# Optimization experiments

Measured on AMD Instinct MI355X. Metric: run time of the kernel, lower is better.

Reference implementation:

```python
import jax, jax.numpy as jnp
import numpy as np

HEADS = 4


def _forward(x_atoms, pos, edge_attr, molecular_features, emb_W, emb_b, mp_W1, mp_b1, mp_W2, mp_b2, ln_g, ln_b, attn_in_w, attn_in_b, attn_out_w, attn_out_b, pool_W, pool_b, mol_gate, lrn_gate, molemb_W1, molemb_b1, molemb_W2, molemb_b2, lrnemb_W1, lrnemb_b1, lrnemb_W2, lrnemb_b2, fus_W1, fus_b1, fus_W2, fus_b2, head_W1, head_b1, head_W2, head_b2, edge_index, batch_idx):
    N = x_atoms.shape[0]
    B = molecular_features.shape[0]
    A = N // B  # equal-size molecules; batch_idx = repeat(arange(B), A)
    H = emb_W.shape[1]
    L = mp_W1.shape[0]
    src, dst = edge_index[0], edge_index[1]  # PyG: x_j = x[src], x_i = x[dst]
    x = x_atoms @ emb_W + emb_b
    # distance features (constant across layers)
    diff = pos[dst] - pos[src]
    d = jnp.sqrt(jnp.sum(diff * diff, axis=1, keepdims=True) + 1e-12)
    dist_feat = jnp.concatenate([d, 1.0 / (1.0 + d), jnp.exp(-d)], axis=1)  # [E,3]
    ones_e = jnp.ones((src.shape[0], 1), x.dtype)
    cnt = jnp.maximum(jax.ops.segment_sum(ones_e, dst, num_segments=N), 1.0)
    for l in range(L):
        res = x
        msg = jnp.concatenate([x[dst], x[src], dist_feat], axis=1)  # [E, 2H+3]
        msg = jax.nn.relu(msg @ mp_W1[l] + mp_b1[l]) @ mp_W2[l] + mp_b2[l]
        x = jax.ops.segment_sum(msg, dst, num_segments=N) / cnt  # mean aggregation
        y = x + res
        mu = y.mean(-1, keepdims=True)
        var = jnp.var(y, axis=-1, keepdims=True)
        x = (y - mu) * jax.lax.rsqrt(var + 1e-5) * ln_g[l] + ln_b[l]
    xm = x.reshape(B, A, H)
    explicit = xm.mean(axis=1)  # scatter_mean over equal-size graphs
    # per-molecule multi-head self-attention (torch MHA, eval mode)
    hd = H // HEADS
    qkv = xm @ attn_in_w.T + attn_in_b
    q, k, v = jnp.split(qkv, 3, axis=-1)
    q = q.reshape(B, A, HEADS, hd)
    k = k.reshape(B, A, HEADS, hd)
    v = v.reshape(B, A, HEADS, hd)
    scores = jnp.einsum('bqhd,bkhd->bhqk', q, k) / jnp.sqrt(jnp.asarray(hd, x.dtype))
    att = jax.nn.softmax(scores, axis=-1)
    o = jnp.einsum('bhqk,bkhd->bqhd', att, v).reshape(B, A, H)
    attended = o @ attn_out_w.T + attn_out_b
    aw = jax.nn.softmax(jnp.sum(attended * xm, axis=-1), axis=1)  # [B,A]
    wmean = jnp.sum(attended * aw[..., None], axis=1)
    maxp = attended.max(axis=1)
    meanp = attended.mean(axis=1)
    stdp = jnp.std(attended, axis=1, ddof=1)  # torch.std unbiased
    pooled = jnp.stack([wmean, maxp, meanp, stdp], axis=0)  # [4,B,H]
    proj = jnp.einsum('kbh,khf->kbf', pooled, pool_W) + pool_b[:, None, :]
    learned = jnp.moveaxis(proj, 0, 1).reshape(B, -1)  # [B,LF]
    # per-property gated MLPs, vectorized over P (atom gates are computed but unused in the source)
    gm = molecular_features[None] * jax.nn.sigmoid(mol_gate)[:, None, :]
    gl = learned[None] * jax.nn.sigmoid(lrn_gate)[:, None, :]
    molrep = jax.nn.relu(jnp.einsum('pbm,pmh->pbh', gm, molemb_W1) + molemb_b1[:, None, :])
    molrep = jnp.einsum('pbh,phk->pbk', molrep, molemb_W2) + molemb_b2[:, None, :]
    lrnrep = jax.nn.relu(jnp.einsum('pbm,pmh->pbh', gl, lrnemb_W1) + lrnemb_b1[:, None, :])
    lrnrep = jnp.einsum('pbh,phk->pbk', lrnrep, lrnemb_W2) + lrnemb_b2[:, None, :]
    P = mol_gate.shape[0]
    comb = jnp.concatenate([jnp.broadcast_to(explicit[None], (P, B, H)), molrep, lrnrep], axis=-1)
    fused = jax.nn.relu(jnp.einsum('pbc,pch->pbh', comb, fus_W1) + fus_b1[:, None, :])
    fused = jnp.einsum('pbh,phk->pbk', fused, fus_W2) + fus_b2[:, None, :]
    h = jax.nn.relu(jnp.einsum('pbh,phk->pbk', fused, head_W1) + head_b1[:, None, :])
    out = jnp.einsum('pbk,pko->pbo', h, head_W2) + head_b2[:, None, :]
    return out  # [P,B,1]: stacked predictions for the 4 properties


def setup_inputs() -> dict:
    key = jax.random.key(0)
    ks = jax.random.split(key, 24)
    B, A, F, M, H, LF, L, P = 1024, 32, 64, 200, 128, 64, 3, 4
    N = B * A
    E = N * 16
    H2, H4, Q = H // 2, H // 4, LF // 4
    n = lambda i, shape, s=1.0: jax.random.normal(ks[i], shape, dtype=jnp.float32) * s
    inp = {}
    inp['x_atoms'] = n(0, (N, F))
    inp['pos'] = n(1, (N, 3)) * 3.0
    inp['edge_attr'] = n(2, (E, 4))
    inp['molecular_features'] = n(3, (B, M))
    inp['emb_W'] = n(4, (F, H), 0.1)
    inp['emb_b'] = jnp.zeros((H,), jnp.float32)
    inp['mp_W1'] = n(5, (L, 2 * H + 3, H), 0.05)
    inp['mp_b1'] = jnp.zeros((L, H), jnp.float32)
    inp['mp_W2'] = n(6, (L, H, H), 0.05)
    inp['mp_b2'] = jnp.zeros((L, H), jnp.float32)
    inp['ln_g'] = jnp.ones((L, H), jnp.float32)
    inp['ln_b'] = jnp.zeros((L, H), jnp.float32)
    inp['attn_in_w'] = n(7, (3 * H, H), 0.08)
    inp['attn_in_b'] = jnp.zeros((3 * H,), jnp.float32)
    inp['attn_out_w'] = n(8, (H, H), 0.08)
    inp['attn_out_b'] = jnp.zeros((H,), jnp.float32)
    inp['pool_W'] = n(9, (4, H, Q), 0.08)
    inp['pool_b'] = jnp.zeros((4, Q), jnp.float32)
    inp['mol_gate'] = n(10, (P, M))
    inp['lrn_gate'] = n(11, (P, LF))
    inp['molemb_W1'] = n(12, (P, M, H2), 0.08)
    inp['molemb_b1'] = jnp.zeros((P, H2), jnp.float32)
    inp['molemb_W2'] = n(13, (P, H2, H2), 0.08)
    inp['molemb_b2'] = jnp.zeros((P, H2), jnp.float32)
    inp['lrnemb_W1'] = n(14, (P, LF, H2), 0.08)
    inp['lrnemb_b1'] = jnp.zeros((P, H2), jnp.float32)
    inp['lrnemb_W2'] = n(15, (P, H2, H2), 0.08)
    inp['lrnemb_b2'] = jnp.zeros((P, H2), jnp.float32)
    inp['fus_W1'] = n(16, (P, 2 * H, H), 0.08)
    inp['fus_b1'] = jnp.zeros((P, H), jnp.float32)
    inp['fus_W2'] = n(17, (P, H, H2), 0.08)
    inp['fus_b2'] = jnp.zeros((P, H2), jnp.float32)
    inp['head_W1'] = n(18, (P, H2, H4), 0.08)
    inp['head_b1'] = jnp.zeros((P, H4), jnp.float32)
    inp['head_W2'] = n(19, (P, H4, 1), 0.08)
    inp['head_b2'] = jnp.zeros((P, 1), jnp.float32)
    inp['edge_index'] = jax.random.randint(ks[20], (2, E), 0, N)
    inp['batch_idx'] = jnp.repeat(jnp.arange(B), A)
    return inp


def reference(x_atoms, pos, edge_attr, molecular_features, emb_W, emb_b, mp_W1, mp_b1, mp_W2, mp_b2, ln_g, ln_b, attn_in_w, attn_in_b, attn_out_w, attn_out_b, pool_W, pool_b, mol_gate, lrn_gate, molemb_W1, molemb_b1, molemb_W2, molemb_b2, lrnemb_W1, lrnemb_b1, lrnemb_W2, lrnemb_b2, fus_W1, fus_b1, fus_W2, fus_b2, head_W1, head_b1, head_W2, head_b2, edge_index, batch_idx):
    return _forward(x_atoms, pos, edge_attr, molecular_features, emb_W, emb_b, mp_W1, mp_b1, mp_W2, mp_b2, ln_g, ln_b, attn_in_w, attn_in_b, attn_out_w, attn_out_b, pool_W, pool_b, mol_gate, lrn_gate, molemb_W1, molemb_b1, molemb_W2, molemb_b2, lrnemb_W1, lrnemb_b1, lrnemb_W2, lrnemb_b2, fus_W1, fus_b1, fus_W2, fus_b2, head_W1, head_b1, head_W2, head_b2, edge_index, batch_idx)
```

## Files before the change

### kernel.cpp

```cpp
#include <hip/hip_runtime.h>

#define NE 524288
#define NN 32768
#define NB 1024

#define F4(p) (*(const float4*)(p))

typedef __bf16 bf16x8 __attribute__((ext_vector_type(8)));
typedef float  f32x4  __attribute__((ext_vector_type(4)));

__device__ __forceinline__ float sigmoidf_(float v) { return 1.f / (1.f + expf(-v)); }

__device__ __forceinline__ void bf16split(float f, short &hi, short &lo) {
  unsigned u = __float_as_uint(f);
  unsigned rh = (u + 0x7FFFu + ((u >> 16) & 1u)) >> 16;
  float fh = __uint_as_float(rh << 16);
  float fl = f - fh;
  unsigned u2 = __float_as_uint(fl);
  unsigned rl = (u2 + 0x7FFFu + ((u2 >> 16) & 1u)) >> 16;
  hi = (short)rh; lo = (short)rl;
}

__device__ __forceinline__ unsigned short f2bf(float f) {
  unsigned u = __float_as_uint(f);
  return (unsigned short)((u + 0x7FFFu + ((u >> 16) & 1u)) >> 16);
}
__device__ __forceinline__ float bf2f(unsigned short h) {
  return __uint_as_float(((unsigned)h) << 16);
}

__device__ __forceinline__ void ld32(float* xr, const float* p) {
#pragma unroll
  for (int i = 0; i < 32; i += 4) {
    float4 v = F4(&p[i]);
    xr[i] = v.x; xr[i+1] = v.y; xr[i+2] = v.z; xr[i+3] = v.w;
  }
}

__device__ __forceinline__ float dot32r(const float* __restrict__ w, const float* xr) {
  float s = 0.f;
#pragma unroll
  for (int i = 0; i < 32; i += 4) {
    float4 ww = F4(&w[i]);
    s = fmaf(xr[i],   ww.x, s);
    s = fmaf(xr[i+1], ww.y, s);
    s = fmaf(xr[i+2], ww.z, s);
    s = fmaf(xr[i+3], ww.w, s);
  }
  return s;
}

__global__ __launch_bounds__(128) void embed_kernel(
    const float* __restrict__ xa, const float* __restrict__ W,
    const float* __restrict__ b, float* __restrict__ x)
{
  __shared__ float a[64];
  const int n = blockIdx.x, t = threadIdx.x;
  if (t < 64) a[t] = xa[n*64 + t];
  __syncthreads();
  float s = b[t];
#pragma unroll 8
  for (int f = 0; f < 64; ++f) s = fmaf(a[f], W[f*128 + t], s);
  x[n*128 + t] = s;
}

__global__ __launch_bounds__(256) void hist_kernel(const int* __restrict__ ei, int* __restrict__ cnt) {
  const int e = blockIdx.x*256 + threadIdx.x;
  atomicAdd(&cnt[ei[NE + e]], 1);
}

__global__ __launch_bounds__(1024) void scan_kernel(
    const int* __restrict__ cnt, int* __restrict__ off, int* __restrict__ cur)
{
  __shared__ int wsum[16];
  const int t = threadIdx.x;
  int local[32];
  const int base = t*32;
  int s = 0;
#pragma unroll
  for (int i = 0; i < 32; ++i) { local[i] = cnt[base+i]; s += local[i]; }
  int pre = s;
  const int lane = t & 63;
#pragma unroll
  for (int o = 1; o < 64; o <<= 1) { int v = __shfl_up(pre, o); if (lane >= o) pre += v; }
  if (lane == 63) wsum[t >> 6] = pre;
  __syncthreads();
  if (t == 0) { int a = 0; for (int w = 0; w < 16; ++w) { int v = wsum[w]; wsum[w] = a; a += v; } }
  __syncthreads();
  int excl = wsum[t >> 6] + pre - s;
#pragma unroll
  for (int i = 0; i < 32; ++i) { off[base+i] = excl; cur[base+i] = excl; excl += local[i]; }
  if (t == 1023) off[NN] = excl;
}

__global__ __launch_bounds__(256) void scatter_kernel(
    const float* __restrict__ pos, const int* __restrict__ ei,
    int* __restrict__ cur, float4* __restrict__ csr_rec)
{
  const int e = blockIdx.x*256 + threadIdx.x;
  const int s = ei[e];
  const int d = ei[NE + e];
  float dx = pos[d*3+0] - pos[s*3+0];
  float dy = pos[d*3+1] - pos[s*3+1];
  float dz = pos[d*3+2] - pos[s*3+2];
  float dist = sqrtf(dx*dx + dy*dy + dz*dz + 1e-12f);
  const int slot = atomicAdd(&cur[d], 1);
  csr_rec[slot] = make_float4(__int_as_float(s), dist, 1.f/(1.f + dist), expf(-dist));
}

__device__ __forceinline__ void pack_decode(int r, int N, int &k, int &n) {
  const int j = r & 7, lane = (r >> 3) & 63, rest = r >> 9;
  const int NT = N >> 4;
  const int t = rest % NT, kc = rest / NT;
  k = kc*32 + (lane >> 4)*8 + j;
  n = t*16 + (lane & 15);
}

#define W1AB_OFF 0
#define W2_OFF   98304
#define WIN_OFF  147456
#define WOUT_OFF 196608
#define HA_OFF   212992
#define HB_OFF   270336
#define HL_OFF   335872
#define HD_OFF   352256
#define HF1_OFF  417792
#define HF2_OFF  942080
#define HH1_OFF  1073152
#define PK_TOTAL 1105920

__global__ __launch_bounds__(256) void prep_kernel(
    const float* __restrict__ mp_W1, const float* __restrict__ mp_W2,
    const float* __restrict__ win, const float* __restrict__ wout,
    const float* __restrict__ mp_b1,
    const float* __restrict__ mol_gate, const float* __restrict__ lrn_gate,
    const float* __restrict__ meW1, const float* __restrict__ meW2,
    const float* __restrict__ leW1, const float* __restrict__ leW2,
    const float* __restrict__ fW1, const float* __restrict__ fW2,
    const float* __restrict__ hW1,
    short* __restrict__ bh, short* __restrict__ bl, float* __restrict__ pqbias)
{
  const int i = blockIdx.x*256 + threadIdx.x;
  if (i < 768) { const int l = i >> 8, t = i & 255; pqbias[i] = t < 128 ? mp_b1[l*128 + t] : 0.f; }
  if (i >= PK_TOTAL) return;
  int k, n; float v;
  if (i < W2_OFF) {
    const int l = i / 32768, r = i % 32768;
    pack_decode(r, 256, k, n);
    const float* W = mp_W1 + (size_t)l*259*128;
    v = (n < 128) ? W[k*128 + n] : W[(128+k)*128 + (n-128)];
  } else if (i < WIN_OFF) {
    const int q = i - W2_OFF, l = q / 16384, r = q % 16384;
    pack_decode(r, 128, k, n);
    v = mp_W2[(size_t)l*16384 + k*128 + n];
  } else if (i < WOUT_OFF) {
    pack_decode(i - WIN_OFF, 384, k, n);
    v = win[n*128 + k];
  } else if (i < HA_OFF) {
    pack_decode(i - WOUT_OFF, 128, k, n);
    v = wout[n*128 + k];
  } else if (i < HB_OFF) {
    pack_decode(i - HA_OFF, 256, k, n);
    const int p = n >> 6, h = n & 63;
    v = (k < 200) ? meW1[p*12800 + k*64 + h] * sigmoidf_(mol_gate[p*200 + k]) : 0.f;
  } else if (i < HL_OFF) {
    pack_decode(i - HB_OFF, 256, k, n);
    const int p = n >> 6, h = n & 63, kp = k >> 6, c = k & 63;
    v = (kp == p) ? meW2[p*4096 + c*64 + h] : 0.f;
  } else if (i < HD_OFF) {
    pack_decode(i - HL_OFF, 256, k, n);
    const int p = n >> 6, h = n & 63;
    v = leW1[p*4096 + k*64 + h] * sigmoidf_(lrn_gate[p*64 + k]);
  } else if (i < HF1_OFF) {
    pack_decode(i - HD_OFF, 256, k, n);
    const int p = n >> 6, h = n & 63, kp = k >> 6, c = k & 63;
    v = (kp == p) ? leW2[p*4096 + c*64 + h] : 0.f;
  } else if (i < HF2_OFF) {
    pack_decode(i - HF1_OFF, 512, k, n);
    const int p = n >> 7, h = n & 127, kp = k >> 8, c = k & 255;
    v = (kp == p) ? fW1[p*32768 + c*128 + h] : 0.f;
  } else if (i < HH1_OFF) {
    pack_decode(i - HF2_OFF, 256, k, n);
    const int p = n >> 6, h = n & 63, kp = k >> 7, c = k & 127;
    v = (kp == p) ? fW2[p*8192 + c*64 + h] : 0.f;
  } else {
    pack_decode(i - HH1_OFF, 128, k, n);
    const int p = n >> 5, h = n & 31, kp = k >> 6, c = k & 63;
    v = (kp == p) ? hW1[p*2048 + c*32 + h] : 0.f;
  }
  short h_, lo; bf16split(v, h_, lo);
  bh[i] = h_; bl[i] = lo;
}

__global__ __launch_bounds__(256, 2) void mfma_gemm_kernel(
    const float* __restrict__ A, int lda, int K,
    const short* __restrict__ Bh, const short* __restrict__ Bl,
    const float* __restrict__ bias, float* __restrict__ C, int ncols, int ldc,
    int colstride, int coloff, int relu,
    unsigned short* __restrict__ qbf)
{
  const int lane = threadIdx.x & 63, wid = threadIdx.x >> 6;
  const int m0 = blockIdx.x * 128 + wid * 32;
  const int n0 = blockIdx.y * 64;
  const int NT = ncols >> 4;
  const int cl = lane & 15, kg = lane >> 4;
  const int KC = K >> 5;

  f32x4 acc[2][4];
#pragma unroll
  for (int s = 0; s < 2; ++s)
#pragma unroll
    for (int t = 0; t < 4; ++t) acc[s][t] = (f32x4){0.f,0.f,0.f,0.f};

  for (int kc = 0; kc < KC; ++kc) {
    bf16x8 Ah[2], Al[2];
#pragma unroll
    for (int s = 0; s < 2; ++s) {
      const float* ap = &A[(size_t)(m0 + s*16 + cl)*lda + kc*32 + kg*8];
      const float4 f0 = F4(ap), f1 = F4(ap + 4);
      const float fv[8] = {f0.x,f0.y,f0.z,f0.w,f1.x,f1.y,f1.z,f1.w};
      union { short s[8]; bf16x8 b; } uh, ul;
#pragma unroll
      for (int j = 0; j < 8; ++j) bf16split(fv[j], uh.s[j], ul.s[j]);
      Ah[s] = uh.b; Al[s] = ul.b;
    }
    bf16x8 Bfh[4], Bfl[4];
#pragma unroll
    for (int t = 0; t < 4; ++t) {
      const size_t off = (((size_t)(kc*NT + (n0 >> 4) + t))*64 + lane)*8;
      Bfh[t] = *(const bf16x8*)&Bh[off];
      Bfl[t] = *(const bf16x8*)&Bl[off];
    }
#pragma unroll
    for (int s = 0; s < 2; ++s)
#pragma unroll
      for (int t = 0; t < 4; ++t)
        acc[s][t] = __builtin_amdgcn_mfma_f32_16x16x32_bf16(Ah[s], Bfh[t], acc[s][t], 0, 0, 0);
#pragma unroll
    for (int s = 0; s < 2; ++s)
#pragma unroll
      for (int t = 0; t < 4; ++t)
        acc[s][t] = __builtin_amdgcn_mfma_f32_16x16x32_bf16(Ah[s], Bfl[t], acc[s][t], 0, 0, 0);
#pragma unroll
    for (int s = 0; s < 2; ++s)
#pragma unroll
      for (int t = 0; t < 4; ++t)
        acc[s][t] = __builtin_amdgcn_mfma_f32_16x16x32_bf16(Al[s], Bfh[t], acc[s][t], 0, 0, 0);
  }

#pragma unroll
  for (int t = 0; t < 4; ++t) {
    const int col = n0 + t*16 + cl;
    const float bv = bias[col];
    const int dstcol = (col >> 6)*colstride + coloff + (col & 63);
#pragma unroll
    for (int s = 0; s < 2; ++s) {
      const int rbase = m0 + s*16 + kg*4;
#pragma unroll
      for (int r = 0; r < 4; ++r) {
        float v = acc[s][t][r] + bv;
        if (relu) v = fmaxf(v, 0.f);
        if (qbf && col >= 128)
          qbf[(size_t)(rbase + r)*128 + (col - 128)] = f2bf(v);
        else
          C[(size_t)(rbase + r)*ldc + dstcol] = v;
      }
    }
  }
}

__global__ __launch_bounds__(256, 2) void mfma_gemm_ln_kernel(
    const float* __restrict__ A, int lda,
    const short* __restrict__ Bh, const short* __restrict__ Bl,
    const float* __restrict__ b2, const int* __restrict__ csr_off,
    const float* __restrict__ g, const float* __restrict__ bb,
    float* __restrict__ x)
{
  const int lane = threadIdx.x & 63, wid = threadIdx.x >> 6;
  const int m0 = blockIdx.x * 64 + wid * 16;
  const int cl = lane & 15, kg = lane >> 4;

  bf16x8 Ah[4], Al[4];
#pragma unroll
  for (int kc = 0; kc < 4; ++kc) {
    const float* ap = &A[(size_t)(m0 + cl)*lda + kc*32 + kg*8];
    const float4 f0 = F4(ap), f1 = F4(ap + 4);
    const float fv[8] = {f0.x,f0.y,f0.z,f0.w,f1.x,f1.y,f1.z,f1.w};
    union { short s[8]; bf16x8 b; } uh, ul;
#pragma unroll
    for (int j = 0; j < 8; ++j) bf16split(fv[j], uh.s[j], ul.s[j]);
    Ah[kc] = uh.b; Al[kc] = ul.b;
  }

  f32x4 acc[8];
#pragma unroll
  for (int t = 0; t < 8; ++t) acc[t] = (f32x4){0.f,0.f,0.f,0.f};

#pragma unroll
  for (int kc = 0; kc < 4; ++kc) {
    bf16x8 Bfh[8], Bfl[8];
#pragma unroll
    for (int t = 0; t < 8; ++t) {
      const size_t off = (((size_t)(kc*8 + t))*64 + lane)*8;
      Bfh[t] = *(const bf16x8*)&Bh[off];
      Bfl[t] = *(const bf16x8*)&Bl[off];
    }
#pragma unroll
    for (int t = 0; t < 8; ++t)
      acc[t] = __builtin_amdgcn_mfma_f32_16x16x32_bf16(Ah[kc], Bfh[t], acc[t], 0, 0, 0);
#pragma unroll
    for (int t = 0; t < 8; ++t)
      acc[t] = __builtin_amdgcn_mfma_f32_16x16x32_bf16(Ah[kc], Bfl[t], acc[t], 0, 0, 0);
#pragma unroll
    for (int t = 0; t < 8; ++t)
      acc[t] = __builtin_amdgcn_mfma_f32_16x16x32_bf16(Al[kc], Bfh[t], acc[t], 0, 0, 0);
  }

  const int r0 = m0 + kg*4;
  float sflag[4];
#pragma unroll
  for (int r = 0; r < 4; ++r)
    sflag[r] = (csr_off[r0 + r + 1] > csr_off[r0 + r]) ? 1.f : 0.f;

  float ps[4] = {0.f,0.f,0.f,0.f}, pq[4] = {0.f,0.f,0.f,0.f};
  float yv[8][4];
#pragma unroll
  for (int t = 0; t < 8; ++t) {
    const int col = t*16 + cl;
    const float b2v = b2[col];
#pragma unroll
    for (int r = 0; r < 4; ++r) {
      const float y = acc[t][r] + sflag[r]*b2v + x[(size_t)(r0 + r)*128 + col];
      yv[t][r] = y;
      ps[r] += y;
      pq[r] = fmaf(y, y, pq[r]);
    }
  }
#pragma unroll
  for (int o = 1; o < 16; o <<= 1) {
#pragma unroll
    for (int r = 0; r < 4; ++r) { ps[r] += __shfl_xor(ps[r], o); pq[r] += __shfl_xor(pq[r], o); }
  }
#pragma unroll
  for (int r = 0; r < 4; ++r) {
    const float mu = ps[r] * (1.f/128.f);
    const float var = pq[r]*(1.f/128.f) - mu*mu;
    const float rstd = rsqrtf(var + 1e-5f);
#pragma unroll
    for (int t = 0; t < 8; ++t) {
      const int col = t*16 + cl;
      x[(size_t)(r0 + r)*128 + col] = (yv[t][r] - mu)*rstd*g[col] + bb[col];
    }
  }
}

__global__ __launch_bounds__(256, 6) void agg_kernel(
    float* __restrict__ P, const unsigned short* __restrict__ Qbf,
    const int* __restrict__ csr_off, const float4* __restrict__ csr_rec,
    const float* __restrict__ W1)
{
  const int tid = threadIdx.x;
  const int node = blockIdx.x*4 + (tid >> 6);
  const int lane = tid & 63;
  const int c0 = lane*2;
  const int off0 = csr_off[node], off1 = csr_off[node+1];

  const float* __restrict__ w1c = W1 + 256*128;
  const float w00 = w1c[c0],       w01 = w1c[c0+1];
  const float w10 = w1c[128+c0],   w11 = w1c[128+c0+1];
  const float w20 = w1c[256+c0],   w21 = w1c[256+c0+1];
  const float2 p = *(const float2*)&P[(size_t)node*128 + c0];

  float a0 = 0.f, a1 = 0.f;
  int e = off0;
  for (; e + 8 <= off1; e += 8) {
    float4 rc[8];
#pragma unroll
    for (int j = 0; j < 8; ++j) rc[j] = csr_rec[e+j];
    ushort2 qv[8];
#pragma unroll
    for (int j = 0; j < 8; ++j)
      qv[j] = *(const ushort2*)&Qbf[(size_t)__float_as_int(rc[j].x)*128 + c0];
#pragma unroll
    for (int j = 0; j < 8; ++j) {
      float h0 = p.x + bf2f(qv[j].x);
      h0 = fmaf(rc[j].y, w00, h0); h0 = fmaf(rc[j].z, w10, h0); h0 = fmaf(rc[j].w, w20, h0);
      float h1 = p.y + bf2f(qv[j].y);
      h1 = fmaf(rc[j].y, w01, h1); h1 = fmaf(rc[j].z, w11, h1); h1 = fmaf(rc[j].w, w21, h1);
      a0 += fmaxf(h0, 0.f);
      a1 += fmaxf(h1, 0.f);
    }
  }
  for (; e < off1; ++e) {
    const float4 rc = csr_rec[e];
    const ushort2 qv = *(const ushort2*)&Qbf[(size_t)__float_as_int(rc.x)*128 + c0];
    float h0 = p.x + bf2f(qv.x);
    h0 = fmaf(rc.y, w00, h0); h0 = fmaf(rc.z, w10, h0); h0 = fmaf(rc.w, w20, h0);
    float h1 = p.y + bf2f(qv.y);
    h1 = fmaf(rc.y, w01, h1); h1 = fmaf(rc.z, w11, h1); h1 = fmaf(rc.w, w21, h1);
    a0 += fmaxf(h0, 0.f);
    a1 += fmaxf(h1, 0.f);
  }
  const int deg = off1 - off0;
  const float rc_ = deg > 0 ? 1.f/(float)deg : 1.f;
  *(float2*)&P[(size_t)node*128 + c0] = make_float2(a0*rc_, a1*rc_);
}

__global__ __launch_bounds__(128) void attn_kernel(float* __restrict__ dqkv)
{
  __shared__ float sk[32*132];
  __shared__ float sv[32*132];
  const int tid = threadIdx.x;
  const int b = blockIdx.x;

  for (int idx = tid; idx < 1024; idx += 128) {
    const int a = idx >> 5, c4 = idx & 31;
    *(float4*)&sk[a*132 + c4*4] = F4(&dqkv[(size_t)(b*32+a)*384 + 128 + c4*4]);
    *(float4*)&sv[a*132 + c4*4] = F4(&dqkv[(size_t)(b*32+a)*384 + 256 + c4*4]);
  }
  __syncthreads();

  const int h = tid >> 5, qr = tid & 31;
  float qreg[32];
  ld32(qreg, &dqkv[(size_t)(b*32+qr)*384 + h*32]);

  float sc[32];
#pragma unroll
  for (int k = 0; k < 32; ++k)
    sc[k] = dot32r(&sk[k*132 + h*32], qreg) * 0.17677669529663687f;
  float mx = sc[0];
#pragma unroll
  for (int k = 1; k < 32; ++k) mx = fmaxf(mx, sc[k]);
  float se = 0.f;
#pragma unroll
  for (int k = 0; k < 32; ++k) { sc[k] = expf(sc[k] - mx); se += sc[k]; }
  const float inv = 1.f / se;

  __syncthreads();

  float od[32];
#pragma unroll
  for (int i = 0; i < 32; ++i) od[i] = 0.f;
#pragma unroll 4
  for (int k = 0; k < 32; ++k) {
    const float w = sc[k] * inv;
    const float* vr = &sv[k*132 + h*32];
#pragma unroll
    for (int i = 0; i < 32; i += 4) {
      float4 v = F4(&vr[i]);
      od[i]   = fmaf(w, v.x, od[i]);
      od[i+1] = fmaf(w, v.y, od[i+1]);
      od[i+2] = fmaf(w, v.z, od[i+2]);
      od[i+3] = fmaf(w, v.w, od[i+3]);
    }
  }
#pragma unroll
  for (int i = 0; i < 32; i += 4)
    *(float4*)&sk[qr*132 + h*32 + i] = make_float4(od[i], od[i+1], od[i+2], od[i+3]);
  __syncthreads();

  for (int idx = tid; idx < 1024; idx += 128) {
    const int a = idx >> 5, c4 = idx & 31;
    *(float4*)&dqkv[(size_t)(b*32+a)*384 + 256 + c4*4] = F4(&sk[a*132 + c4*4]);
  }
}

__global__ __launch_bounds__(128) void pool_kernel(
    const float* __restrict__ att, const float* __restrict__ x,
    const float* __restrict__ pW, const float* __restrict__ pb,
    float* __restrict__ expl, float* __restrict__ lrn, float* __restrict__ comb)
{
  __shared__ float satt[32*132];
  __shared__ float sx[32*132];
  __shared__ float aw_l[32];
  __shared__ float spool[512];
  const int tid = threadIdx.x;
  const int b = blockIdx.x;

  for (int idx = tid; idx < 1024; idx += 128) {
    const int a = idx >> 5, c4 = idx & 31;
    *(float4*)&satt[a*132 + c4*4] = F4(&att[(size_t)(b*32+a)*128 + c4*4]);
    *(float4*)&sx[a*132 + c4*4]   = F4(&x[(size_t)(b*32+a)*128 + c4*4]);
  }
  __syncthreads();

  {
    const int a = tid >> 2, q4 = tid & 3;
    float sp = 0.f;
#pragma unroll
    for (int i = 0; i < 32; ++i)
      sp = fmaf(satt[a*132 + q4*32 + i], sx[a*132 + q4*32 + i], sp);
    sp += __shfl_xor(sp, 1);
    sp += __shfl_xor(sp, 2);
    if (q4 == 0) aw_l[a] = sp;
  }
  __syncthreads();

  {
    float awr[32];
    float mxl = aw_l[0];
#pragma unroll
    for (int a = 1; a < 32; ++a) mxl = fmaxf(mxl, aw_l[a]);
    float se = 0.f;
#pragma unroll
    for (int a = 0; a < 32; ++a) { awr[a] = expf(aw_l[a] - mxl); se += awr[a]; }
    const float inv = 1.f / se;
    const int c = tid;
    float mx = -3.4e38f, sm = 0.f, wm = 0.f, ex = 0.f;
#pragma unroll
    for (int a = 0; a < 32; ++a) {
      const float v = satt[a*132 + c];
      mx = fmaxf(mx, v);
      sm += v;
      wm = fmaf(v, awr[a], wm);
      ex += sx[a*132 + c];
    }
    wm *= inv;
    const float mean = sm * 0.03125f;
    float s2 = 0.f;
#pragma unroll
    for (int a = 0; a < 32; ++a) {
      const float d = satt[a*132 + c] - mean;
      s2 = fmaf(d, d, s2);
    }
    const float stdp = sqrtf(s2 * (1.f/31.f));
    const float exm = ex * 0.03125f;
    expl[b*128 + c] = exm;
#pragma unroll
    for (int p = 0; p < 4; ++p)
      comb[(size_t)b*1024 + p*256 + c] = exm;
    spool[c]       = wm;
    spool[128 + c] = mx;
    spool[256 + c] = mean;
    spool[384 + c] = stdp;
  }
  __syncthreads();

  if (tid < 64) {
    const int k = tid >> 4, qq = tid & 15;
    const float* pk = pW + k*2048;
    float s0 = 0.f, s1 = 0.f, s2 = 0.f, s3 = 0.f;
    for (int h2 = 0; h2 < 128; h2 += 4) {
      s0 = fmaf(spool[k*128 + h2],   pk[h2*16 + qq],     s0);
      s1 = fmaf(spool[k*128 + h2+1], pk[(h2+1)*16 + qq], s1);
      s2 = fmaf(spool[k*128 + h2+2], pk[(h2+2)*16 + qq], s2);
      s3 = fmaf(spool[k*128 + h2+3], pk[(h2+3)*16 + qq], s3);
    }
    lrn[b*64 + tid] = pb[k*16 + qq] + (s0+s1) + (s2+s3);
  }
}

__global__ __launch_bounds__(256) void padmolf_kernel(
    const float* __restrict__ molf, float* __restrict__ mp)
{
  const int i = blockIdx.x*256 + threadIdx.x;
  const int b = i / 224, m = i - b*224;
  mp[i] = (m < 200) ? molf[b*200 + m] : 0.f;
}

__global__ __launch_bounds__(256) void outdot_kernel(
    const float* __restrict__ H1, const float* __restrict__ hW2,
    const float* __restrict__ hb2, float* __restrict__ out)
{
  const int id = blockIdx.x*256 + threadIdx.x;
  const int b = id & 1023, p = id >> 10;
  const float* hp = &H1[(size_t)b*128 + p*32];
  const float* wp = &hW2[p*32];
  float s0=0.f,s1=0.f,s2=0.f,s3=0.f;
  for (int h = 0; h < 32; h += 4) {
    s0 = fmaf(hp[h],   wp[h],   s0);
    s1 = fmaf(hp[h+1], wp[h+1], s1);
    s2 = fmaf(hp[h+2], wp[h+2], s2);
    s3 = fmaf(hp[h+3], wp[h+3], s3);
  }
  out[p*1024 + b] = (s0+s1) + (s2+s3) + hb2[p];
}

extern "C" void kernel_launch(void* const* d_in, const int* in_sizes, int n_in,
                              void* d_out, int out_size, void* d_ws, size_t ws_size,
                              hipStream_t stream) {
  const float* x_atoms    = (const float*)d_in[0];
  const float* pos        = (const float*)d_in[1];
  const float* molf       = (const float*)d_in[3];
  const float* emb_W      = (const float*)d_in[4];
  const float* emb_b      = (const float*)d_in[5];
  const float* mp_W1      = (const float*)d_in[6];
  const float* mp_b1      = (const float*)d_in[7];
  const float* mp_W2      = (const float*)d_in[8];
  const float* mp_b2      = (const float*)d_in[9];
  const float* ln_g       = (const float*)d_in[10];
  const float* ln_b       = (const float*)d_in[11];
  const float* attn_in_w  = (const float*)d_in[12];
  const float* attn_in_b  = (const float*)d_in[13];
  const float* attn_out_w = (const float*)d_in[14];
  const float* attn_out_b = (const float*)d_in[15];
  const float* pool_W     = (const float*)d_in[16];
  const float* pool_b     = (const float*)d_in[17];
  const float* mol_gate   = (const float*)d_in[18];
  const float* lrn_gate   = (const float*)d_in[19];
  const float* meW1       = (const float*)d_in[20];
  const float* meb1       = (const float*)d_in[21];
  const float* meW2       = (const float*)d_in[22];
  const float* meb2       = (const float*)d_in[23];
  const float* leW1       = (const float*)d_in[24];
  const float* leb1       = (const float*)d_in[25];
  const float* leW2       = (const float*)d_in[26];
  const float* leb2       = (const float*)d_in[27];
  const float* fW1        = (const float*)d_in[28];
  const float* fb1        = (const float*)d_in[29];
  const float* fW2        = (const float*)d_in[30];
  const float* fb2        = (const float*)d_in[31];
  const float* hW1        = (const float*)d_in[32];
  const float* hb1        = (const float*)d_in[33];
  const float* hW2        = (const float*)d_in[34];
  const float* hb2        = (const float*)d_in[35];
  const int*   ei         = (const int*)d_in[36];

  float* ws      = (float*)d_ws;
  float* x       = ws;
  float* region  = x + (size_t)NN*128;
  float* P       = region;
  unsigned short* Qbf = (unsigned short*)(region + (size_t)NN*128);
  float* dqkv    = region;
  float* att     = region + (size_t)NN*384;
  float* csr_rf  = att + (size_t)NN*128;
  float4* csr_rec = (float4*)csr_rf;
  int*   cnt_i   = (int*)(csr_rf + (size_t)NE*4);
  int*   csr_off = cnt_i + NN;
  int*   cur     = csr_off + NN + 64;
  float* lrn     = (float*)(cur + NN);
  float* expl    = lrn + NB*64;
  float* pqbias  = expl + NB*128;
  short* bh      = (short*)(pqbias + 768);
  short* bl      = bh + PK_TOTAL;

  float* molfPad = region;
  float* MOLR1   = region + 229376;
  float* LRNR1   = region + 491520;
  float* COMB    = region + 753664;
  float* FUS1    = region + 1802240;
  float* FUS2    = region + 2326528;
  float* H1      = region + 2588672;

  hipMemsetAsync(cnt_i, 0, (size_t)NN*sizeof(int), stream);

  embed_kernel<<<NN, 128, 0, stream>>>(x_atoms, emb_W, emb_b, x);
  hist_kernel<<<NE/256, 256, 0, stream>>>(ei, cnt_i);
  scan_kernel<<<1, 1024, 0, stream>>>(cnt_i, csr_off, cur);
  scatter_kernel<<<NE/256, 256, 0, stream>>>(pos, ei, cur, csr_rec);
  prep_kernel<<<(PK_TOTAL + 255)/256, 256, 0, stream>>>(
      mp_W1, mp_W2, attn_in_w, attn_out_w, mp_b1,
      mol_gate, lrn_gate, meW1, meW2, leW1, leW2, fW1, fW2, hW1,
      bh, bl, pqbias);

  for (int l = 0; l < 3; ++l) {
    mfma_gemm_kernel<<<dim3(NN/128, 4), 256, 0, stream>>>(
        x, 128, 128, bh + W1AB_OFF + l*32768, bl + W1AB_OFF + l*32768,
        pqbias + l*256, P, 256, 128, 64, 0, 0, Qbf);
    agg_kernel<<<NN/4, 256, 0, stream>>>(P, Qbf, csr_off, csr_rec,
                                         mp_W1 + (size_t)l*259*128);
    mfma_gemm_ln_kernel<<<NN/64, 256, 0, stream>>>(
        P, 128, bh + W2_OFF + l*16384, bl + W2_OFF + l*16384,
        mp_b2 + l*128, csr_off, ln_g + l*128, ln_b + l*128, x);
  }

  mfma_gemm_kernel<<<dim3(NN/128, 6), 256, 0, stream>>>(
      x, 128, 128, bh + WIN_OFF, bl + WIN_OFF, attn_in_b, dqkv, 384, 384, 64, 0, 0, nullptr);
  attn_kernel<<<NB, 128, 0, stream>>>(dqkv);
  mfma_gemm_kernel<<<dim3(NN/128, 2), 256, 0, stream>>>(
      dqkv + 256, 384, 128, bh + WOUT_OFF, bl + WOUT_OFF, attn_out_b, att, 128, 128, 64, 0, 0, nullptr);
  pool_kernel<<<NB, 128, 0, stream>>>(att, x, pool_W, pool_b, expl, lrn, COMB);

  padmolf_kernel<<<(1024*224)/256, 256, 0, stream>>>(molf, molfPad);
  mfma_gemm_kernel<<<dim3(8, 4), 256, 0, stream>>>(
      molfPad, 224, 224, bh + HA_OFF, bl + HA_OFF, meb1, MOLR1, 256, 256, 64, 0, 1, nullptr);
  mfma_gemm_kernel<<<dim3(8, 4), 256, 0, stream>>>(
      MOLR1, 256, 256, bh + HB_OFF, bl + HB_OFF, meb2, COMB, 256, 1024, 256, 128, 0, nullptr);
  mfma_gemm_kernel<<<dim3(8, 4), 256, 0, stream>>>(
      lrn, 64, 64, bh + HL_OFF, bl + HL_OFF, leb1, LRNR1, 256, 256, 64, 0, 1, nullptr);
  mfma_gemm_kernel<<<dim3(8, 4), 256, 0, stream>>>(
      LRNR1, 256, 256, bh + HD_OFF, bl + HD_OFF, leb2, COMB, 256, 1024, 256, 192, 0, nullptr);
  mfma_gemm_kernel<<<dim3(8, 8), 256, 0, stream>>>(
      COMB, 1024, 1024, bh + HF1_OFF, bl + HF1_OFF, fb1, FUS1, 512, 512, 64, 0, 1, nullptr);
  mfma_gemm_kernel<<<dim3(8, 4), 256, 0, stream>>>(
      FUS1, 512, 512, bh + HF2_OFF, bl + HF2_OFF, fb2, FUS2, 256, 256, 64, 0, 0, nullptr);
  mfma_gemm_kernel<<<dim3(8, 2), 256, 0, stream>>>(
      FUS2, 256, 256, bh + HH1_OFF, bl + HH1_OFF, hb1, H1, 128, 128, 64, 0, 1, nullptr);
  outdot_kernel<<<16, 256, 0, stream>>>(H1, hW2, hb2, (float*)d_out);
}
```

Measured before the change: 472.5 us.

## Fuse per-molecule MLP head chain into one kernel and embed via MFMA GEMM

Replaces the padmolf kernel, seven small block-diagonal MFMA GEMM launches and the outdot kernel with one fused_head_kernel. Each block handles 32 molecules for one head, keeps intermediates in shared memory and does FP32 FMAs straight from the unpacked weights, so it no longer computes the zero blocks. The embedding projection moves from a per-atom scalar kernel to the split-bf16 MFMA GEMM, with emb_W added to the weight pre-pack. The pre-pack shrinks because the head weights are no longer packed. The trade-off is that the fused head runs only 128 blocks of scalar FMAs, which may limit parallelism.

Measured after the change: 447.1 us. 1.06x faster.

```diff
diff --git a/kernel.cpp b/kernel.cpp
--- a/kernel.cpp
+++ b/kernel.cpp
@@ -48,20 +48,6 @@
     s = fmaf(xr[i+3], ww.w, s);
   }
   return s;
-}
-
-__global__ __launch_bounds__(128) void embed_kernel(
-    const float* __restrict__ xa, const float* __restrict__ W,
-    const float* __restrict__ b, float* __restrict__ x)
-{
-  __shared__ float a[64];
-  const int n = blockIdx.x, t = threadIdx.x;
-  if (t < 64) a[t] = xa[n*64 + t];
-  __syncthreads();
-  float s = b[t];
-#pragma unroll 8
-  for (int f = 0; f < 64; ++f) s = fmaf(a[f], W[f*128 + t], s);
-  x[n*128 + t] = s;
 }
 
 __global__ __launch_bounds__(256) void hist_kernel(const int* __restrict__ ei, int* __restrict__ cnt) {
@@ -120,24 +106,13 @@
 #define W2_OFF   98304
 #define WIN_OFF  147456
 #define WOUT_OFF 196608
-#define HA_OFF   212992
-#define HB_OFF   270336
-#define HL_OFF   335872
-#define HD_OFF   352256
-#define HF1_OFF  417792
-#define HF2_OFF  942080
-#define HH1_OFF  1073152
-#define PK_TOTAL 1105920
+#define EMB_OFF  212992
+#define PK_TOTAL 221184
 
 __global__ __launch_bounds__(256) void prep_kernel(
     const float* __restrict__ mp_W1, const float* __restrict__ mp_W2,
     const float* __restrict__ win, const float* __restrict__ wout,
-    const float* __restrict__ mp_b1,
-    const float* __restrict__ mol_gate, const float* __restrict__ lrn_gate,
-    const float* __restrict__ meW1, const float* __restrict__ meW2,
-    const float* __restrict__ leW1, const float* __restrict__ leW2,
-    const float* __restrict__ fW1, const float* __restrict__ fW2,
-    const float* __restrict__ hW1,
+    const float* __restrict__ emb_W, const float* __restrict__ mp_b1,
     short* __restrict__ bh, short* __restrict__ bl, float* __restrict__ pqbias)
 {
   const int i = blockIdx.x*256 + threadIdx.x;
@@ -156,37 +131,12 @@
   } else if (i < WOUT_OFF) {
     pack_decode(i - WIN_OFF, 384, k, n);
     v = win[n*128 + k];
-  } else if (i < HA_OFF) {
+  } else if (i < EMB_OFF) {
     pack_decode(i - WOUT_OFF, 128, k, n);
     v = wout[n*128 + k];
-  } else if (i < HB_OFF) {
-    pack_decode(i - HA_OFF, 256, k, n);
-    const int p = n >> 6, h = n & 63;
-    v = (k < 200) ? meW1[p*12800 + k*64 + h] * sigmoidf_(mol_gate[p*200 + k]) : 0.f;
-  } else if (i < HL_OFF) {
-    pack_decode(i - HB_OFF, 256, k, n);
-    const int p = n >> 6, h = n & 63, kp = k >> 6, c = k & 63;
-    v = (kp == p) ? meW2[p*4096 + c*64 + h] : 0.f;
-  } else if (i < HD_OFF) {
-    pack_decode(i - HL_OFF, 256, k, n);
-    const int p = n >> 6, h = n & 63;
-    v = leW1[p*4096 + k*64 + h] * sigmoidf_(lrn_gate[p*64 + k]);
-  } else if (i < HF1_OFF) {
-    pack_decode(i - HD_OFF, 256, k, n);
-    const int p = n >> 6, h = n & 63, kp = k >> 6, c = k & 63;
-    v = (kp == p) ? leW2[p*4096 + c*64 + h] : 0.f;
-  } else if (i < HF2_OFF) {
-    pack_decode(i - HF1_OFF, 512, k, n);
-    const int p = n >> 7, h = n & 127, kp = k >> 8, c = k & 255;
-    v = (kp == p) ? fW1[p*32768 + c*128 + h] : 0.f;
-  } else if (i < HH1_OFF) {
-    pack_decode(i - HF2_OFF, 256, k, n);
-    const int p = n >> 6, h = n & 63, kp = k >> 7, c = k & 127;
-    v = (kp == p) ? fW2[p*8192 + c*64 + h] : 0.f;
   } else {
-    pack_decode(i - HH1_OFF, 128, k, n);
-    const int p = n >> 5, h = n & 31, kp = k >> 6, c = k & 63;
-    v = (kp == p) ? hW1[p*2048 + c*32 + h] : 0.f;
+    pack_decode(i - EMB_OFF, 128, k, n);
+    v = emb_W[k*128 + n];
   }
   short h_, lo; bf16split(v, h_, lo);
   bh[i] = h_; bl[i] = lo;
@@ -196,8 +146,7 @@
     const float* __restrict__ A, int lda, int K,
     const short* __restrict__ Bh, const short* __restrict__ Bl,
     const float* __restrict__ bias, float* __restrict__ C, int ncols, int ldc,
-    int colstride, int coloff, int relu,
-    unsigned short* __restrict__ qbf)
+    int relu, unsigned short* __restrict__ qbf)
 {
   const int lane = threadIdx.x & 63, wid = threadIdx.x >> 6;
   const int m0 = blockIdx.x * 128 + wid * 32;
@@ -252,7 +201,6 @@
   for (int t = 0; t < 4; ++t) {
     const int col = n0 + t*16 + cl;
     const float bv = bias[col];
-    const int dstcol = (col >> 6)*colstride + coloff + (col & 63);
 #pragma unroll
     for (int s = 0; s < 2; ++s) {
       const int rbase = m0 + s*16 + kg*4;
@@ -263,7 +211,7 @@
         if (qbf && col >= 128)
           qbf[(size_t)(rbase + r)*128 + (col - 128)] = f2bf(v);
         else
-          C[(size_t)(rbase + r)*ldc + dstcol] = v;
+          C[(size_t)(rbase + r)*ldc + col] = v;
       }
     }
   }
@@ -468,7 +416,7 @@
 __global__ __launch_bounds__(128) void pool_kernel(
     const float* __restrict__ att, const float* __restrict__ x,
     const float* __restrict__ pW, const float* __restrict__ pb,
-    float* __restrict__ expl, float* __restrict__ lrn, float* __restrict__ comb)
+    float* __restrict__ expl, float* __restrict__ lrn)
 {
   __shared__ float satt[32*132];
   __shared__ float sx[32*132];
@@ -524,11 +472,7 @@
       s2 = fmaf(d, d, s2);
     }
     const float stdp = sqrtf(s2 * (1.f/31.f));
-    const float exm = ex * 0.03125f;
-    expl[b*128 + c] = exm;
-#pragma unroll
-    for (int p = 0; p < 4; ++p)
-      comb[(size_t)b*1024 + p*256 + c] = exm;
+    expl[b*128 + c] = ex * 0.03125f;
     spool[c]       = wm;
     spool[128 + c] = mx;
     spool[256 + c] = mean;
@@ -550,30 +494,175 @@
   }
 }
 
-__global__ __launch_bounds__(256) void padmolf_kernel(
-    const float* __restrict__ molf, float* __restrict__ mp)
-{
-  const int i = blockIdx.x*256 + threadIdx.x;
-  const int b = i / 224, m = i - b*224;
-  mp[i] = (m < 200) ? molf[b*200 + m] : 0.f;
-}
-
-__global__ __launch_bounds__(256) void outdot_kernel(
-    const float* __restrict__ H1, const float* __restrict__ hW2,
-    const float* __restrict__ hb2, float* __restrict__ out)
-{
-  const int id = blockIdx.x*256 + threadIdx.x;
-  const int b = id & 1023, p = id >> 10;
-  const float* hp = &H1[(size_t)b*128 + p*32];
-  const float* wp = &hW2[p*32];
-  float s0=0.f,s1=0.f,s2=0.f,s3=0.f;
-  for (int h = 0; h < 32; h += 4) {
-    s0 = fmaf(hp[h],   wp[h],   s0);
-    s1 = fmaf(hp[h+1], wp[h+1], s1);
-    s2 = fmaf(hp[h+2], wp[h+2], s2);
-    s3 = fmaf(hp[h+3], wp[h+3], s3);
-  }
-  out[p*1024 + b] = (s0+s1) + (s2+s3) + hb2[p];
+__global__ __launch_bounds__(256) void fused_head_kernel(
+    const float* __restrict__ molf, const float* __restrict__ lrn,
+    const float* __restrict__ expl,
+    const float* __restrict__ mol_gate, const float* __restrict__ lrn_gate,
+    const float* __restrict__ meW1, const float* __restrict__ meb1,
+    const float* __restrict__ meW2, const float* __restrict__ meb2,
+    const float* __restrict__ leW1, const float* __restrict__ leb1,
+    const float* __restrict__ leW2, const float* __restrict__ leb2,
+    const float* __restrict__ fW1, const float* __restrict__ fb1,
+    const float* __restrict__ fW2, const float* __restrict__ fb2,
+    const float* __restrict__ hW1, const float* __restrict__ hb1,
+    const float* __restrict__ hW2, const float* __restrict__ hb2,
+    float* __restrict__ out)
+{
+  const int p  = blockIdx.y;
+  const int b0 = blockIdx.x * 32;
+  const int t  = threadIdx.x;
+  const int m  = t >> 3, hg = t & 7;
+
+  __shared__ float sgm[32][201];
+  __shared__ float sgl[32][65];
+  __shared__ float smr[32][65];
+  __shared__ float slr[32][65];
+  __shared__ float scomb[32][257];
+  __shared__ float sf1[32][129];
+  __shared__ float sf2[32][65];
+
+  for (int i = t; i < 32*200; i += 256) {
+    const int mm = i / 200, k = i - mm*200;
+    sgm[mm][k] = molf[(size_t)(b0+mm)*200 + k] * sigmoidf_(mol_gate[p*200 + k]);
+  }
+  for (int i = t; i < 32*64; i += 256) {
+    const int mm = i >> 6, k = i & 63;
+    sgl[mm][k] = lrn[(size_t)(b0+mm)*64 + k] * sigmoidf_(lrn_gate[p*64 + k]);
+  }
+  for (int i = t; i < 32*128; i += 256) {
+    const int mm = i >> 7, c = i & 127;
+    scomb[mm][c] = expl[(size_t)(b0+mm)*128 + c];
+  }
+  __syncthreads();
+
+  {
+    const float* w = meW1 + p*12800;
+    const int h0 = hg*8;
+    float acc[8] = {0.f,0.f,0.f,0.f,0.f,0.f,0.f,0.f};
+    for (int k = 0; k < 200; ++k) {
+      const float a = sgm[m][k];
+      const float4 w0 = F4(&w[k*64 + h0]);
+      const float4 w1 = F4(&w[k*64 + h0 + 4]);
+      acc[0] = fmaf(a, w0.x, acc[0]); acc[1] = fmaf(a, w0.y, acc[1]);
+      acc[2] = fmaf(a, w0.z, acc[2]); acc[3] = fmaf(a, w0.w, acc[3]);
+      acc[4] = fmaf(a, w1.x, acc[4]); acc[5] = fmaf(a, w1.y, acc[5]);
+      acc[6] = fmaf(a, w1.z, acc[6]); acc[7] = fmaf(a, w1.w, acc[7]);
+    }
+#pragma unroll
+    for (int j = 0; j < 8; ++j)
+      smr[m][h0+j] = fmaxf(acc[j] + meb1[p*64 + h0 + j], 0.f);
+  }
+  {
+    const float* w = leW1 + p*4096;
+    const int h0 = hg*8;
+    float acc[8] = {0.f,0.f,0.f,0.f,0.f,0.f,0.f,0.f};
+    for (int k = 0; k < 64; ++k) {
+      const float a = sgl[m][k];
+      const float4 w0 = F4(&w[k*64 + h0]);
+      const float4 w1 = F4(&w[k*64 + h0 + 4]);
+      acc[0] = fmaf(a, w0.x, acc[0]); acc[1] = fmaf(a, w0.y, acc[1]);
+      acc[2] = fmaf(a, w0.z, acc[2]); acc[3] = fmaf(a, w0.w, acc[3]);
+      acc[4] = fmaf(a, w1.x, acc[4]); acc[5] = fmaf(a, w1.y, acc[5]);
+      acc[6] = fmaf(a, w1.z, acc[6]); acc[7] = fmaf(a, w1.w, acc[7]);
+    }
+#pragma unroll
+    for (int j = 0; j < 8; ++j)
+      slr[m][h0+j] = fmaxf(acc[j] + leb1[p*64 + h0 + j], 0.f);
+  }
+  __syncthreads();
+
+  {
+    const float* w  = meW2 + p*4096;
+    const float* w2 = leW2 + p*4096;
+    const int h0 = hg*8;
+    float acc[8] = {0.f,0.f,0.f,0.f,0.f,0.f,0.f,0.f};
+    float bcc[8] = {0.f,0.f,0.f,0.f,0.f,0.f,0.f,0.f};
+    for (int k = 0; k < 64; ++k) {
+      const float a = smr[m][k];
+      const float b = slr[m][k];
+      const float4 w0 = F4(&w[k*64 + h0]);
+      const float4 w1 = F4(&w[k*64 + h0 + 4]);
+      const float4 v0 = F4(&w2[k*64 + h0]);
+      const float4 v1 = F4(&w2[k*64 + h0 + 4]);
+      acc[0] = fmaf(a, w0.x, acc[0]); acc[1] = fmaf(a, w0.y, acc[1]);
+      acc[2] = fmaf(a, w0.z, acc[2]); acc[3] = fmaf(a, w0.w, acc[3]);
+      acc[4] = fmaf(a, w1.x, acc[4]); acc[5] = fmaf(a, w1.y, acc[5]);
+      acc[6] = fmaf(a, w1.z, acc[6]); acc[7] = fmaf(a, w1.w, acc[7]);
+      bcc[0] = fmaf(b, v0.x, bcc[0]); bcc[1] = fmaf(b, v0.y, bcc[1]);
+      bcc[2] = fmaf(b, v0.z, bcc[2]); bcc[3] = fmaf(b, v0.w, bcc[3]);
+      bcc[4] = fmaf(b, v1.x, bcc[4]); bcc[5] = fmaf(b, v1.y, bcc[5]);
+      bcc[6] = fmaf(b, v1.z, bcc[6]); bcc[7] = fmaf(b, v1.w, bcc[7]);
+    }
+#pragma unroll
+    for (int j = 0; j < 8; ++j) {
+      scomb[m][128 + h0 + j] = acc[j] + meb2[p*64 + h0 + j];
+      scomb[m][192 + h0 + j] = bcc[j] + leb2[p*64 + h0 + j];
+    }
+  }
+  __syncthreads();
+
+  {
+    const float* w = fW1 + p*32768;
+    const int h0 = hg*16;
+    float acc[16];
+#pragma unroll
+    for (int j = 0; j < 16; ++j) acc[j] = 0.f;
+    for (int k = 0; k < 256; ++k) {
+      const float a = scomb[m][k];
+      const float* wp = &w[k*128 + h0];
+#pragma unroll
+      for (int j = 0; j < 16; j += 4) {
+        const float4 wv = F4(&wp[j]);
+        acc[j]   = fmaf(a, wv.x, acc[j]);
+        acc[j+1] = fmaf(a, wv.y, acc[j+1]);
+        acc[j+2] = fmaf(a, wv.z, acc[j+2]);
+        acc[j+3] = fmaf(a, wv.w, acc[j+3]);
+      }
+    }
+#pragma unroll
+    for (int j = 0; j < 16; ++j)
+      sf1[m][h0+j] = fmaxf(acc[j] + fb1[p*128 + h0 + j], 0.f);
+  }
+  __syncthreads();
+
+  {
+    const float* w = fW2 + p*8192;
+    const int h0 = hg*8;
+    float acc[8] = {0.f,0.f,0.f,0.f,0.f,0.f,0.f,0.f};
+    for (int k = 0; k < 128; ++k) {
+      const float a = sf1[m][k];
+      const float4 w0 = F4(&w[k*64 + h0]);
+      const float4 w1 = F4(&w[k*64 + h0 + 4]);
+      acc[0] = fmaf(a, w0.x, acc[0]); acc[1] = fmaf(a, w0.y, acc[1]);
+      acc[2] = fmaf(a, w0.z, acc[2]); acc[3] = fmaf(a, w0.w, acc[3]);
+      acc[4] = fmaf(a, w1.x, acc[4]); acc[5] = fmaf(a, w1.y, acc[5]);
+      acc[6] = fmaf(a, w1.z, acc[6]); acc[7] = fmaf(a, w1.w, acc[7]);
+    }
+#pragma unroll
+    for (int j = 0; j < 8; ++j)
+      sf2[m][h0+j] = acc[j] + fb2[p*64 + h0 + j];
+  }
+  __syncthreads();
+
+  {
+    const float* w = hW1 + p*2048;
+    const int h0 = hg*4;
+    float acc[4] = {0.f,0.f,0.f,0.f};
+    for (int k = 0; k < 64; ++k) {
+      const float a = sf2[m][k];
+      const float4 w0 = F4(&w[k*32 + h0]);
+      acc[0] = fmaf(a, w0.x, acc[0]); acc[1] = fmaf(a, w0.y, acc[1]);
+      acc[2] = fmaf(a, w0.z, acc[2]); acc[3] = fmaf(a, w0.w, acc[3]);
+    }
+    float val = 0.f;
+#pragma unroll
+    for (int j = 0; j < 4; ++j)
+      val = fmaf(fmaxf(acc[j] + hb1[p*32 + h0 + j], 0.f), hW2[p*32 + h0 + j], val);
+    val += __shfl_xor(val, 1);
+    val += __shfl_xor(val, 2);
+    val += __shfl_xor(val, 4);
+    if (hg == 0) out[p*1024 + b0 + m] = val + hb2[p];
+  }
 }
 
 extern "C" void kernel_launch(void* const* d_in, const int* in_sizes, int n_in,
@@ -634,29 +723,21 @@
   short* bh      = (short*)(pqbias + 768);
   short* bl      = bh + PK_TOTAL;
 
-  float* molfPad = region;
-  float* MOLR1   = region + 229376;
-  float* LRNR1   = region + 491520;
-  float* COMB    = region + 753664;
-  float* FUS1    = region + 1802240;
-  float* FUS2    = region + 2326528;
-  float* H1      = region + 2588672;
-
   hipMemsetAsync(cnt_i, 0, (size_t)NN*sizeof(int), stream);
 
-  embed_kernel<<<NN, 128, 0, stream>>>(x_atoms, emb_W, emb_b, x);
+  prep_kernel<<<(PK_TOTAL + 255)/256, 256, 0, stream>>>(
+      mp_W1, mp_W2, attn_in_w, attn_out_w, emb_W, mp_b1, bh, bl, pqbias);
   hist_kernel<<<NE/256, 256, 0, stream>>>(ei, cnt_i);
   scan_kernel<<<1, 1024, 0, stream>>>(cnt_i, csr_off, cur);
   scatter_kernel<<<NE/256, 256, 0, stream>>>(pos, ei, cur, csr_rec);
-  prep_kernel<<<(PK_TOTAL + 255)/256, 256, 0, stream>>>(
-      mp_W1, mp_W2, attn_in_w, attn_out_w, mp_b1,
-      mol_gate, lrn_gate, meW1, meW2, leW1, leW2, fW1, fW2, hW1,
-      bh, bl, pqbias);
+
+  mfma_gemm_kernel<<<dim3(NN/128, 2), 256, 0, stream>>>(
+      x_atoms, 64, 64, bh + EMB_OFF, bl + EMB_OFF, emb_b, x, 128, 128, 0, nullptr);
 
   for (int l = 0; l < 3; ++l) {
     mfma_gemm_kernel<<<dim3(NN/128, 4), 256, 0, stream>>>(
         x, 128, 128, bh + W1AB_OFF + l*32768, bl + W1AB_OFF + l*32768,
-        pqbias + l*256, P, 256, 128, 64, 0, 0, Qbf);
+        pqbias + l*256, P, 256, 128, 0, Qbf);
     agg_kernel<<<NN/4, 256, 0, stream>>>(P, Qbf, csr_off, csr_rec,
                                          mp_W1 + (size_t)l*259*128);
     mfma_gemm_ln_kernel<<<NN/64, 256, 0, stream>>>(
@@ -665,26 +746,14 @@
   }
 
   mfma_gemm_kernel<<<dim3(NN/128, 6), 256, 0, stream>>>(
-      x, 128, 128, bh + WIN_OFF, bl + WIN_OFF, attn_in_b, dqkv, 384, 384, 64, 0, 0, nullptr);
+      x, 128, 128, bh + WIN_OFF, bl + WIN_OFF, attn_in_b, dqkv, 384, 384, 0, nullptr);
   attn_kernel<<<NB, 128, 0, stream>>>(dqkv);
   mfma_gemm_kernel<<<dim3(NN/128, 2), 256, 0, stream>>>(
-      dqkv + 256, 384, 128, bh + WOUT_OFF, bl + WOUT_OFF, attn_out_b, att, 128, 128, 64, 0, 0, nullptr);
-  pool_kernel<<<NB, 128, 0, stream>>>(att, x, pool_W, pool_b, expl, lrn, COMB);
-
-  padmolf_kernel<<<(1024*224)/256, 256, 0, stream>>>(molf, molfPad);
-  mfma_gemm_kernel<<<dim3(8, 4), 256, 0, stream>>>(
-      molfPad, 224, 224, bh + HA_OFF, bl + HA_OFF, meb1, MOLR1, 256, 256, 64, 0, 1, nullptr);
-  mfma_gemm_kernel<<<dim3(8, 4), 256, 0, stream>>>(
-      MOLR1, 256, 256, bh + HB_OFF, bl + HB_OFF, meb2, COMB, 256, 1024, 256, 128, 0, nullptr);
-  mfma_gemm_kernel<<<dim3(8, 4), 256, 0, stream>>>(
-      lrn, 64, 64, bh + HL_OFF, bl + HL_OFF, leb1, LRNR1, 256, 256, 64, 0, 1, nullptr);
-  mfma_gemm_kernel<<<dim3(8, 4), 256, 0, stream>>>(
-      LRNR1, 256, 256, bh + HD_OFF, bl + HD_OFF, leb2, COMB, 256, 1024, 256, 192, 0, nullptr);
-  mfma_gemm_kernel<<<dim3(8, 8), 256, 0, stream>>>(
-      COMB, 1024, 1024, bh + HF1_OFF, bl + HF1_OFF, fb1, FUS1, 512, 512, 64, 0, 1, nullptr);
-  mfma_gemm_kernel<<<dim3(8, 4), 256, 0, stream>>>(
-      FUS1, 512, 512, bh + HF2_OFF, bl + HF2_OFF, fb2, FUS2, 256, 256, 64, 0, 0, nullptr);
-  mfma_gemm_kernel<<<dim3(8, 2), 256, 0, stream>>>(
-      FUS2, 256, 256, bh + HH1_OFF, bl + HH1_OFF, hb1, H1, 128, 128, 64, 0, 1, nullptr);
-  outdot_kernel<<<16, 256, 0, stream>>>(H1, hW2, hb2, (float*)d_out);
-}
+      dqkv + 256, 384, 128, bh + WOUT_OFF, bl + WOUT_OFF, attn_out_b, att, 128, 128, 0, nullptr);
+  pool_kernel<<<NB, 128, 0, stream>>>(att, x, pool_W, pool_b, expl, lrn);
+
+  fused_head_kernel<<<dim3(32, 4), 256, 0, stream>>>(
+      molf, lrn, expl, mol_gate, lrn_gate,
+      meW1, meb1, meW2, meb2, leW1, leb1, leW2, leb2,
+      fW1, fb1, fW2, fb2, hW1, hb1, hW2, hb2, (float*)d_out);
+}
```
